# Performance work log

Hardware: AMD Instinct MI355X
Metric: run time of the kernel (lower is better)

Reference implementation:

```python
import jax, jax.numpy as jnp
import numpy as np

N, E, B, M = 50000, 100000, 50, 50
NPG = N // B            # atoms per graph
DIN, H1, H2, DE, AAF, G = 32, 32, 64, 16, 95, 128
K, T = 3, 6             # ARMA num_stacks, num_layers
F1, F2, F3 = 64, 32, 16
EA = 2 * (M - 1)        # amino-acid edges per graph


def setup_inputs() -> dict:
    key = jax.random.key(0)
    ks = jax.random.split(key, 24)
    s = 0.05
    def w(k, shape):
        return jax.random.normal(k, shape, jnp.float32) * s
    return {
        "x": jax.random.normal(ks[0], (N, DIN), jnp.float32),
        "edge_attr": jax.random.normal(ks[1], (E, DE), jnp.float32),
        "aa_features": jax.random.normal(ks[2], (B, M, AAF), jnp.float32),
        "edge_index": jax.random.randint(ks[3], (2, E), 0, N),
        "monomer_labels": jax.random.randint(ks[4], (B, NPG), 0, M),
        "amino_edge_index": jax.random.randint(ks[5], (2, EA), 0, M),
        "W_e1": w(ks[6], (DE, DIN * H1)), "b_e1": jnp.zeros((DIN * H1,), jnp.float32),
        "root1": w(ks[7], (DIN, H1)), "bias1": jnp.zeros((H1,), jnp.float32),
        "W_e2": w(ks[8], (DE, H1 * H2)), "b_e2": jnp.zeros((H1 * H2,), jnp.float32),
        "root2": w(ks[9], (H1, H2)), "bias2": jnp.zeros((H2,), jnp.float32),
        "Wa_atom": w(ks[10], (H2, 1)), "ba_atom": jnp.zeros((1,), jnp.float32),
        "arma_init_w": w(ks[11], (K, H2 + AAF, G)),
        "arma_w": w(ks[12], (T - 1, K, G, G)),
        "arma_root_w": w(ks[13], (T, K, H2 + AAF, G)),
        "arma_bias": jnp.zeros((T, K, G), jnp.float32),
        "Wa_aa": w(ks[14], (G, 1)), "ba_aa": jnp.zeros((1,), jnp.float32),
        "W1": w(ks[15], (G, F1)), "b1": jnp.zeros((F1,), jnp.float32),
        "W2": w(ks[16], (F1, F2)), "b2": jnp.zeros((F2,), jnp.float32),
        "W3": w(ks[17], (F2, F3)), "b3": jnp.zeros((F3,), jnp.float32),
        "W4": w(ks[18], (F3, 1)), "b4": jnp.zeros((1,), jnp.float32),
    }


def _nnconv(h, src, dst, edge_attr, Wm, bm, root, bias, fin, fout):
    # NNConv (aggr='add'): edge MLP -> per-edge weight matrix, gather-matmul-scatter
    w_e = (edge_attr @ Wm + bm).reshape(-1, fin, fout)            # [E, fin, fout]
    msg = jnp.einsum('ef,efo->eo', h[src], w_e)                   # [E, fout]
    agg = jax.ops.segment_sum(msg, dst, num_segments=h.shape[0])  # scatter-add to targets
    return agg + h @ root + bias


def _forward(x, edge_attr, aa_features, W_e1, b_e1, root1, bias1, W_e2, b_e2, root2, bias2,
             Wa_atom, ba_atom, arma_init_w, arma_w, arma_root_w, arma_bias, Wa_aa, ba_aa,
             W1, b1, W2, b2, W3, b3, W4, b4, edge_index, monomer_labels, amino_edge_index):
    src, dst = edge_index[0], edge_index[1]
    h = jax.nn.relu(_nnconv(x, src, dst, edge_attr, W_e1, b_e1, root1, bias1, DIN, H1))
    h = jax.nn.relu(_nnconv(h, src, dst, edge_attr, W_e2, b_e2, root2, bias2, H1, H2))

    # per-graph attention readout over atoms -> amino-acid embeddings (scatter by monomer label)
    xg = h.reshape(B, NPG, H2)
    attn = jax.nn.softmax(xg @ Wa_atom + ba_atom, axis=1)         # softmax over atoms in graph
    wx = xg * attn
    aa = jax.vmap(lambda wxi, lbl: jax.ops.segment_sum(wxi, lbl, num_segments=M))(wx, monomer_labels)
    h_aa = jnp.concatenate([aa, aa_features], axis=-1)            # [B, M, H2+95]

    # ARMAConv: gcn_norm without self-loops on amino-acid graph (shared across graphs)
    asrc, adst = amino_edge_index[0], amino_edge_index[1]
    deg = jax.ops.segment_sum(jnp.ones((EA,), x.dtype), adst, num_segments=M)
    dinv = jnp.where(deg > 0, 1.0 / jnp.sqrt(jnp.maximum(deg, 1.0)), 0.0)
    norm = dinv[asrc] * dinv[adst]                                # [EA]

    def arma(x0):  # x0: [M, H2+95]
        out = jnp.einsum('mf,kfo->kmo', x0, arma_init_w)          # [K, M, G]
        for t in range(T):
            if t > 0:
                out = jnp.einsum('kmo,kop->kmp', out, arma_w[t - 1])
            msg = out[:, asrc] * norm[None, :, None]              # [K, EA, G]
            prop = jax.vmap(lambda m: jax.ops.segment_sum(m, adst, num_segments=M))(msg)
            rootc = jnp.einsum('mf,kfo->kmo', x0, arma_root_w[t])
            out = jax.nn.relu(prop + rootc + arma_bias[t][:, None, :])
        return out.mean(axis=0)                                   # mean over stacks -> [M, G]

    g = jax.vmap(arma)(h_aa)                                      # [B, M, G]

    # attention readout over amino acids
    attn2 = jax.nn.softmax(g @ Wa_aa + ba_aa, axis=1)
    p = jnp.sum(g * attn2, axis=1)                                # [B, G]

    p = jax.nn.relu(p @ W1 + b1)
    p = jax.nn.relu(p @ W2 + b2)
    p = jax.nn.relu(p @ W3 + b3)
    p = p @ W4 + b4
    return p.reshape(-1)                                          # [B]


def reference(x, edge_attr, aa_features, edge_index, monomer_labels, amino_edge_index,
              W_e1, b_e1, root1, bias1, W_e2, b_e2, root2, bias2, Wa_atom, ba_atom,
              arma_init_w, arma_w, arma_root_w, arma_bias, Wa_aa, ba_aa,
              W1, b1, W2, b2, W3, b3, W4, b4):
    return _forward(x, edge_attr, aa_features, W_e1, b_e1, root1, bias1, W_e2, b_e2, root2, bias2,
                    Wa_atom, ba_atom, arma_init_w, arma_w, arma_root_w, arma_bias, Wa_aa, ba_aa,
                    W1, b1, W2, b2, W3, b3, W4, b4, edge_index, monomer_labels, amino_edge_index)
```

## Files before the change

### kernel.cpp

```cpp
#include <hip/hip_runtime.h>
#include <math.h>

#define N_ATOMS 50000
#define E_EDGES 100000
#define B_G     50
#define M_M     50
#define NPG     1000
#define DIN     32
#define H1C     32
#define H2C     64
#define DEC     16
#define AAF     95
#define G_DIM   128
#define K_ST    3
#define T_L     6
#define EA_E    98
#define XDIM    159
#define NS      21
#define MPAD    64
#define GP      132
#define GPS     136
#define KP2     168
#define KW      544
#define SLC     10
#define APB     100
#define NSB     ((N_ATOMS + 255) / 256)

#define OFF_WE2 (H1C * KW)
#define OFF_WT  (OFF_WE2 + H2C * KW)
#define OFF_AW  (OFF_WT + NS * XDIM * G_DIM)
#define OFF_DEG (OFF_AW + (T_L - 1) * K_ST * G_DIM * G_DIM)
#define PREP_TOTAL (OFF_DEG + E_EDGES)

typedef __attribute__((ext_vector_type(8))) short bf16x8;
typedef __attribute__((ext_vector_type(4))) float f32x4;
typedef __attribute__((ext_vector_type(4))) unsigned int u32x4;

__device__ __forceinline__ short f2bf(float f) {
    unsigned int u = __float_as_uint(f);
    unsigned int r = (u + 0x7FFFu + ((u >> 16) & 1u)) >> 16;
    return (short)r;
}
__device__ __forceinline__ float bf2f(short b) {
    return __uint_as_float(((unsigned int)(unsigned short)b) << 16);
}
__device__ __forceinline__ unsigned int cvtpk_bf16(float lo, float hi) {
    unsigned int r;
    asm("v_cvt_pk_bf16_f32 %0, %1, %2" : "=v"(r) : "v"(lo), "v"(hi));
    return r;
}

__device__ __forceinline__ void f4fma(float4& d, float s, const float4& v) {
    d.x += s * v.x; d.y += s * v.y; d.z += s * v.z; d.w += s * v.w;
}
__device__ __forceinline__ void f4add(float4& d, const float4& v) {
    d.x += v.x; d.y += v.y; d.z += v.z; d.w += v.w;
}
__device__ __forceinline__ void f4relu(float4& d) {
    d.x = fmaxf(d.x, 0.f); d.y = fmaxf(d.y, 0.f);
    d.z = fmaxf(d.z, 0.f); d.w = fmaxf(d.w, 0.f);
}

__global__ __launch_bounds__(256) void prep_all(
    const float* __restrict__ We1, const float* __restrict__ be1, short* __restrict__ WB1,
    const float* __restrict__ We2, const float* __restrict__ be2, short* __restrict__ WB2,
    const float* __restrict__ init_w, const float* __restrict__ root_w, short* __restrict__ Wtb,
    const float* __restrict__ arma_w, short* __restrict__ Wab,
    const int* __restrict__ eidx, int* __restrict__ deg,
    const int* __restrict__ aei, int* __restrict__ aa_off,
    int* __restrict__ aa_src, float* __restrict__ aa_nrm)
{
    int tid = threadIdx.x;
    if (blockIdx.x == 0) {
        __shared__ int   sdeg[M_M];
        __shared__ int   scur[M_M];
        __shared__ float sdinv[M_M];
        __shared__ int   soff[M_M + 1];
        if (tid < M_M) { sdeg[tid] = 0; scur[tid] = 0; }
        __syncthreads();
        if (tid < EA_E) atomicAdd(&sdeg[aei[EA_E + tid]], 1);
        __syncthreads();
        if (tid < M_M) {
            float dv = (float)sdeg[tid];
            sdinv[tid] = (dv > 0.f) ? (1.f / sqrtf(fmaxf(dv, 1.f))) : 0.f;
        }
        __syncthreads();
        if (tid == 0) {
            soff[0] = 0;
            for (int m = 0; m < M_M; ++m) soff[m + 1] = soff[m] + sdeg[m];
        }
        __syncthreads();
        if (tid < EA_E) {
            int ss = aei[tid], dd = aei[EA_E + tid];
            int pos = atomicAdd(&scur[dd], 1);
            int idx = soff[dd] + pos;
            aa_src[idx] = ss;
            aa_nrm[idx] = sdinv[ss] * sdinv[dd];
        }
        if (tid < M_M + 1) aa_off[tid] = soff[tid];
        return;
    }
    int idx = (blockIdx.x - 1) * 256 + tid;
    if (idx < OFF_WE2) {
        int o = idx / KW, k = idx - o * KW;
        float v = (k < 512) ? We1[(size_t)k * H1C + o]
                            : be1[(size_t)(k - 512) * H1C + o];
        WB1[idx] = f2bf(v);
    } else if (idx < OFF_WT) {
        int rem = idx - OFF_WE2;
        int o = rem / KW, k = rem - o * KW;
        float v = (k < 512) ? We2[(size_t)k * H2C + o]
                            : be2[(size_t)(k - 512) * H2C + o];
        WB2[rem] = f2bf(v);
    } else if (idx < OFF_AW) {
        int rem = idx - OFF_WT;
        int s = rem / (XDIM * G_DIM);
        int r2 = rem - s * XDIM * G_DIM;
        int k = r2 / G_DIM, n = r2 - k * G_DIM;
        float v = (s < K_ST) ? init_w[rem]
                             : root_w[(size_t)(s - K_ST) * XDIM * G_DIM + r2];
        Wtb[(size_t)s * G_DIM * KP2 + n * KP2 + k] = f2bf(v);
    } else if (idx < OFF_DEG) {
        int rem = idx - OFF_AW;
        int slot = rem / (G_DIM * G_DIM);
        int r2 = rem - slot * G_DIM * G_DIM;
        int p = r2 / G_DIM, n = r2 - p * G_DIM;
        Wab[(size_t)slot * G_DIM * G_DIM + n * G_DIM + p] = f2bf(arma_w[rem]);
    } else if (idx < PREP_TOTAL) {
        int e = idx - OFF_DEG;
        atomicAdd(&deg[eidx[E_EDGES + e]], 1);
    }
}

__global__ __launch_bounds__(256) void scan_part(const int* __restrict__ deg,
                                                 int* __restrict__ bsum)
{
    __shared__ int tmp[256];
    int tid = threadIdx.x;
    int n = blockIdx.x * 256 + tid;
    tmp[tid] = (n < N_ATOMS) ? deg[n] : 0;
    __syncthreads();
    for (int off = 128; off > 0; off >>= 1) {
        if (tid < off) tmp[tid] += tmp[tid + off];
        __syncthreads();
    }
    if (tid == 0) bsum[blockIdx.x] = tmp[0];
}

__global__ __launch_bounds__(256) void scan_mid(const int* __restrict__ bsum,
                                                int* __restrict__ bpre)
{
    __shared__ int tmp[256];
    int tid = threadIdx.x;
    int v = (tid < NSB) ? bsum[tid] : 0;
    tmp[tid] = v;
    __syncthreads();
    for (int off = 1; off < 256; off <<= 1) {
        int t = tmp[tid];
        int add = (tid >= off) ? tmp[tid - off] : 0;
        __syncthreads();
        tmp[tid] = t + add;
        __syncthreads();
    }
    if (tid < NSB) bpre[tid] = tmp[tid] - v;
}

__global__ __launch_bounds__(256) void scan_out(int* __restrict__ deg_off,
                                                const int* __restrict__ bpre)
{
    __shared__ int tmp[256];
    int tid = threadIdx.x;
    int n = blockIdx.x * 256 + tid;
    int v = (n < N_ATOMS) ? deg_off[n] : 0;
    tmp[tid] = v;
    __syncthreads();
    for (int off = 1; off < 256; off <<= 1) {
        int t = tmp[tid];
        int add = (tid >= off) ? tmp[tid - off] : 0;
        __syncthreads();
        tmp[tid] = t + add;
        __syncthreads();
    }
    int incl = tmp[tid];
    int base = bpre[blockIdx.x];
    if (n < N_ATOMS) deg_off[n] = base + incl - v;
    if (n == N_ATOMS - 1) deg_off[N_ATOMS] = base + incl;
}

template<int FOUT, int NTT, int WGRP, int MTB, bool CIPOS>
__global__ __launch_bounds__(256) void edge_msg_v2(
    const float* __restrict__ h, const float* __restrict__ ea,
    const int* __restrict__ eidx, int* __restrict__ ipos,
    const int* __restrict__ off, int* __restrict__ cursor,
    const short* __restrict__ WB, float* __restrict__ msg)
{
    constexpr int KS = 17;
    __shared__ int iplds[MTB * 16];
    int tid  = threadIdx.x;
    int lane = tid & 63, wave = tid >> 6;
    int l16  = lane & 15, quad = lane >> 4;
    int nt   = wave % NTT, tg = wave / NTT;
    int ebase = blockIdx.x * (MTB * 16);

    if (CIPOS) {
        if (tid < MTB * 16) {
            int e = ebase + tid;
            if (e < E_EDGES) {
                int d = eidx[E_EDGES + e];
                int pos = atomicAdd(&cursor[d], 1);
                int p = off[d] + pos;
                iplds[tid] = p;
                ipos[e] = p;
            }
        }
    }

    bf16x8 Bfr[KS];
    {
        const short* wb = WB + (size_t)(nt * 16 + l16) * KW;
        #pragma unroll
        for (int ks = 0; ks < KS; ++ks)
            Bfr[ks] = *(const bf16x8*)(wb + ks * 32 + quad * 8);
    }
    if (CIPOS) __syncthreads();

    for (int t = tg; t < MTB; t += WGRP) {
        int e  = ebase + t * 16 + l16;
        int es = (e < E_EDGES) ? e : (E_EDGES - 1);
        int s  = eidx[es];
        float4 h0 = *(const float4*)(h + (size_t)s * 32 + quad * 8);
        float4 h1 = *(const float4*)(h + (size_t)s * 32 + quad * 8 + 4);
        float hf[8] = {h0.x, h0.y, h0.z, h0.w, h1.x, h1.y, h1.z, h1.w};
        float4 e0 = *(const float4*)(ea + (size_t)es * DEC);
        float4 e1 = *(const float4*)(ea + (size_t)es * DEC + 4);
        float4 e2 = *(const float4*)(ea + (size_t)es * DEC + 8);
        float4 e3 = *(const float4*)(ea + (size_t)es * DEC + 12);
        float eaf[16] = {e0.x, e0.y, e0.z, e0.w, e1.x, e1.y, e1.z, e1.w,
                         e2.x, e2.y, e2.z, e2.w, e3.x, e3.y, e3.z, e3.w};

        f32x4 acc = (f32x4){0.f, 0.f, 0.f, 0.f};
        #pragma unroll
        for (int ks = 0; ks < KS; ++ks) {
            u32x4 av;
            if (ks < DEC) {
                float fac = eaf[ks];
                #pragma unroll
                for (int j = 0; j < 4; ++j)
                    av[j] = cvtpk_bf16(fac * hf[2 * j], fac * hf[2 * j + 1]);
            } else {
                #pragma unroll
                for (int j = 0; j < 4; ++j)
                    av[j] = cvtpk_bf16(hf[2 * j], hf[2 * j + 1]);
            }
            bf16x8 a = __builtin_bit_cast(bf16x8, av);
            acc = __builtin_amdgcn_mfma_f32_16x16x32_bf16(a, Bfr[ks], acc, 0, 0, 0);
        }
        int erb = ebase + t * 16 + quad * 4;
        #pragma unroll
        for (int r = 0; r < 4; ++r) {
            int ee = erb + r;
            if (ee < E_EDGES) {
                int p = CIPOS ? iplds[t * 16 + quad * 4 + r] : ipos[ee];
                msg[(size_t)p * FOUT + nt * 16 + l16] = acc[r];
            }
        }
    }
}

template<int FIN, int FOUT, bool SCORE>
__global__ __launch_bounds__(256) void gather_update(
    const float* __restrict__ msg, const int* __restrict__ off,
    const float* __restrict__ hin,
    const float* __restrict__ root, const float* __restrict__ bias,
    float* __restrict__ hout,
    const float* __restrict__ wa, const float* __restrict__ ba,
    float* __restrict__ sc)
{
    constexpr int NPB = 256 / FOUT;
    __shared__ float rlds[FIN][FOUT];
    __shared__ float hlds[NPB][FIN];
    int tid = threadIdx.x;
    for (int i = tid; i < FIN * FOUT / 4; i += 256) {
        *(float4*)&rlds[0][i * 4] = *(const float4*)(root + i * 4);
    }
    int nb = blockIdx.x * NPB;
    for (int i = tid; i < NPB * FIN; i += 256) {
        int ln = i / FIN, f = i % FIN;
        int n = nb + ln;
        hlds[ln][f] = (n < N_ATOMS) ? hin[(size_t)n * FIN + f] : 0.f;
    }
    __syncthreads();

    int ln = tid / FOUT, o = tid % FOUT;
    int n = nb + ln;
    if (n >= N_ATOMS) return;
    float acc = bias[o];
    #pragma unroll 8
    for (int f = 0; f < FIN; ++f) acc += hlds[ln][f] * rlds[f][o];
    int j0 = off[n], j1 = off[n + 1];
    for (int j = j0; j < j1; ++j) {
        acc += msg[(size_t)j * FOUT + o];
    }
    float hv = fmaxf(acc, 0.f);
    hout[(size_t)n * FOUT + o] = hv;
    if constexpr (SCORE) {
        static_assert(FOUT == 64, "score fusion needs node==wave");
        float sv = hv * wa[o];
        #pragma unroll
        for (int d = 32; d > 0; d >>= 1) sv += __shfl_down(sv, d);
        if (o == 0) sc[n] = sv + ba[0];
    }
}

__global__ __launch_bounds__(256) void atom_scatter_sm(
    const float* __restrict__ h2, const float* __restrict__ sc,
    const int* __restrict__ labels, float* __restrict__ partial)
{
    __shared__ float aa4[4][M_M][H2C];
    __shared__ float red[256];
    int b = blockIdx.x / SLC, s = blockIdx.x % SLC;
    int tid = threadIdx.x;
    int wave = tid >> 6, lane = tid & 63;
    const float* sb = sc + (size_t)b * NPG;

    for (int i = tid; i < 4 * M_M * H2C; i += 256) ((float*)aa4)[i] = 0.f;

    float lmax = -1e30f;
    for (int n = tid; n < NPG; n += 256) lmax = fmaxf(lmax, sb[n]);
    red[tid] = lmax;
    __syncthreads();
    for (int off = 128; off > 0; off >>= 1) {
        if (tid < off) red[tid] = fmaxf(red[tid], red[tid + off]);
        __syncthreads();
    }
    float mx = red[0];
    __syncthreads();
    float lsum = 0.f;
    for (int n = tid; n < NPG; n += 256) lsum += expf(sb[n] - mx);
    red[tid] = lsum;
    __syncthreads();
    for (int off = 128; off > 0; off >>= 1) {
        if (tid < off) red[tid] += red[tid + off];
        __syncthreads();
    }
    float inv = 1.f / red[0];
    __syncthreads();

    int nbase = s * APB;
    const float* hb = h2 + (size_t)b * NPG * H2C;
    #pragma unroll 5
    for (int it = 0; it < APB / 4; ++it) {
        int n = nbase + it * 4 + wave;
        int lbl = labels[b * NPG + n];
        float w = expf(sb[n] - mx) * inv;
        float hv = hb[(size_t)n * H2C + lane];
        aa4[wave][lbl][lane] += hv * w;
    }
    __syncthreads();
    float* pb = partial + (size_t)(b * SLC + s) * M_M * H2C;
    for (int i = tid; i < M_M * H2C; i += 256) {
        float v = ((float*)aa4)[i] + ((float*)aa4)[M_M * H2C + i]
                + ((float*)aa4)[2 * M_M * H2C + i] + ((float*)aa4)[3 * M_M * H2C + i];
        pb[i] = v;
    }
}

__global__ __launch_bounds__(256) void x0_finalize(
    const float* __restrict__ partial, const float* __restrict__ aaf,
    short* __restrict__ x0b)
{
    int idx = blockIdx.x * 256 + threadIdx.x;
    if (idx >= B_G * MPAD * KP2) return;
    int b = idx / (MPAD * KP2);
    int rem = idx - b * (MPAD * KP2);
    int m = rem / KP2, k = rem - m * KP2;
    float v = 0.f;
    if (m < M_M) {
        if (k < H2C) {
            const float* pb = partial + (size_t)b * SLC * M_M * H2C + m * H2C + k;
            #pragma unroll
            for (int s = 0; s < SLC; ++s) v += pb[(size_t)s * (M_M * H2C)];
        } else if (k < XDIM) {
            v = aaf[((size_t)b * M_M + m) * AAF + (k - H2C)];
        }
    }
    x0b[idx] = f2bf(v);
}

__global__ __launch_bounds__(256) void rc_gemm_mfma(
    const short* __restrict__ x0b, const short* __restrict__ Wtb,
    float* __restrict__ RC)
{
    int b = blockIdx.x / NS, s = blockIdx.x % NS;
    int tid = threadIdx.x;
    int lane = tid & 63, wave = tid >> 6;
    int l16 = lane & 15, quad = lane >> 4;
    const short* xa = x0b + (size_t)b * MPAD * KP2 + (wave * 16 + l16) * KP2;
    const short* wb = Wtb + (size_t)s * G_DIM * KP2;

    f32x4 acc[8];
    #pragma unroll
    for (int nt = 0; nt < 8; ++nt) acc[nt] = (f32x4){0.f, 0.f, 0.f, 0.f};

    #pragma unroll
    for (int ks = 0; ks < 5; ++ks) {
        bf16x8 a = *(const bf16x8*)(xa + ks * 32 + quad * 8);
        #pragma unroll
        for (int nt = 0; nt < 8; ++nt) {
            bf16x8 bf = *(const bf16x8*)(wb + (nt * 16 + l16) * KP2 + ks * 32 + quad * 8);
            acc[nt] = __builtin_amdgcn_mfma_f32_16x16x32_bf16(a, bf, acc[nt], 0, 0, 0);
        }
    }
    float* op = RC + (size_t)(b * NS + s) * M_M * G_DIM;
    #pragma unroll
    for (int nt = 0; nt < 8; ++nt) {
        #pragma unroll
        for (int r = 0; r < 4; ++r) {
            int m = wave * 16 + quad * 4 + r;
            if (m < M_M)
                op[m * G_DIM + nt * 16 + l16] = acc[nt][r];
        }
    }
}

__global__ __launch_bounds__(512) void arma_iter(
    const float* __restrict__ RC, const short* __restrict__ Wab,
    const float* __restrict__ arma_bias,
    const int* __restrict__ aa_off, const int* __restrict__ aa_src,
    const float* __restrict__ aa_nrm, float* __restrict__ gfull)
{
    __shared__ float Abuf[MPAD][GP];
    __shared__ float Bbuf[MPAD][GP];
    __shared__ short Bb16[MPAD][GPS];
    __shared__ int   s_off[M_M + 1];
    __shared__ int   s_src[EA_E];
    __shared__ float s_nrm[EA_E];
    int b = blockIdx.x / K_ST, k = blockIdx.x % K_ST;
    int tid = threadIdx.x;
    int oi = tid & 15, mi = tid >> 4;
    int c0 = oi * 4, c1 = 64 + oi * 4;
    int lane = tid & 63, wave = tid >> 6;
    int l16 = lane & 15, quad = lane >> 4;
    int mt = wave >> 1, nh = wave & 1;

    const float* rcb = RC + (size_t)b * NS * M_M * G_DIM;
    if (tid < M_M + 1) s_off[tid] = aa_off[tid];
    if (tid < EA_E) { s_src[tid] = aa_src[tid]; s_nrm[tid] = aa_nrm[tid]; }

    for (int i = tid; i < MPAD * G_DIM; i += 512) {
        int m = i >> 7, o = i & 127;
        Abuf[m][o] = (m < M_M) ? rcb[(size_t)k * M_M * G_DIM + i] : 0.f;
    }
    for (int i = tid; i < MPAD * GPS / 2; i += 512) {
        ((int*)Bb16)[i] = 0;
    }
    __syncthreads();

    for (int t = 0; t < T_L; ++t) {
        if (t > 0) {
            const short* aw = Wab + (size_t)((t - 1) * K_ST + k) * G_DIM * G_DIM;
            f32x4 acc[4];
            #pragma unroll
            for (int nt = 0; nt < 4; ++nt) acc[nt] = (f32x4){0.f, 0.f, 0.f, 0.f};
            #pragma unroll
            for (int ks = 0; ks < 4; ++ks) {
                bf16x8 a = *(const bf16x8*)&Bb16[mt * 16 + l16][ks * 32 + quad * 8];
                #pragma unroll
                for (int nt = 0; nt < 4; ++nt) {
                    int n0 = (nh * 4 + nt) * 16 + l16;
                    bf16x8 bf = *(const bf16x8*)(aw + n0 * G_DIM + ks * 32 + quad * 8);
                    acc[nt] = __builtin_amdgcn_mfma_f32_16x16x32_bf16(a, bf, acc[nt], 0, 0, 0);
                }
            }
            #pragma unroll
            for (int nt = 0; nt < 4; ++nt) {
                #pragma unroll
                for (int r = 0; r < 4; ++r) {
                    Abuf[mt * 16 + quad * 4 + r][(nh * 4 + nt) * 16 + l16] = acc[nt][r];
                }
            }
            __syncthreads();
        }
        const float* rct = rcb + (size_t)(K_ST + t * K_ST + k) * M_M * G_DIM;
        const float* bb  = arma_bias + ((size_t)t * K_ST + k) * G_DIM;
        float4 bias0 = *(const float4*)(bb + c0);
        float4 bias1 = *(const float4*)(bb + c1);
        #pragma unroll
        for (int r = 0; r < 2; ++r) {
            int m = mi * 2 + r;
            if (m < M_M) {
                const float* rr = rct + (size_t)m * G_DIM;
                float4 v0 = bias0, v1 = bias1;
                f4add(v0, *(const float4*)(rr + c0));
                f4add(v1, *(const float4*)(rr + c1));
                int j0 = s_off[m], j1 = s_off[m + 1];
                for (int j = j0; j < j1; ++j) {
                    float nv = s_nrm[j];
                    const float* ap = &Abuf[s_src[j]][0];
                    f4fma(v0, nv, *(const float4*)(ap + c0));
                    f4fma(v1, nv, *(const float4*)(ap + c1));
                }
                f4relu(v0);
                f4relu(v1);
                *(float4*)&Bbuf[m][c0] = v0;
                *(float4*)&Bbuf[m][c1] = v1;
                unsigned int p0 = cvtpk_bf16(v0.x, v0.y);
                unsigned int p1 = cvtpk_bf16(v0.z, v0.w);
                unsigned int p2 = cvtpk_bf16(v1.x, v1.y);
                unsigned int p3 = cvtpk_bf16(v1.z, v1.w);
                *(uint2*)&Bb16[m][c0] = make_uint2(p0, p1);
                *(uint2*)&Bb16[m][c1] = make_uint2(p2, p3);
            }
        }
        __syncthreads();
    }
    float* gb = gfull + ((size_t)(b * K_ST + k)) * M_M * G_DIM;
    for (int i = tid; i < M_M * G_DIM; i += 512) {
        int m = i >> 7, o = i & 127;
        gb[i] = Bbuf[m][o];
    }
}

__global__ __launch_bounds__(128) void aa_readout_mlp(
    const float* __restrict__ gfull, const float* __restrict__ wa,
    const float* __restrict__ ba,
    const float* __restrict__ W1, const float* __restrict__ b1,
    const float* __restrict__ W2, const float* __restrict__ b2,
    const float* __restrict__ W3, const float* __restrict__ b3,
    const float* __restrict__ W4, const float* __restrict__ b4,
    float* __restrict__ out)
{
    __shared__ float g[M_M][G_DIM + 1];
    __shared__ float s2[M_M];
    __shared__ float p[G_DIM];
    __shared__ float r1[64], r2[32], r3[16];
    int b = blockIdx.x, tid = threadIdx.x;
    const float* g0 = gfull + (size_t)b * K_ST * M_M * G_DIM;
    for (int i = tid; i < M_M * G_DIM; i += 128) {
        int m = i >> 7, o = i & 127;
        g[m][o] = (g0[i] + g0[M_M*G_DIM + i] + g0[2*M_M*G_DIM + i]) * (1.f/3.f);
    }
    __syncthreads();
    if (tid < M_M) {
        float sv = ba[0];
        for (int o = 0; o < G_DIM; ++o) sv += g[tid][o] * wa[o];
        s2[tid] = sv;
    }
    __syncthreads();
    if (tid == 0) {
        float mx = -1e30f;
        for (int m = 0; m < M_M; ++m) mx = fmaxf(mx, s2[m]);
        float den = 0.f;
        for (int m = 0; m < M_M; ++m) den += expf(s2[m] - mx);
        float inv = 1.f / den;
        for (int m = 0; m < M_M; ++m) s2[m] = expf(s2[m] - mx) * inv;
    }
    __syncthreads();
    {
        float pv = 0.f;
        for (int m = 0; m < M_M; ++m) pv += g[m][tid] * s2[m];
        p[tid] = pv;
    }
    __syncthreads();
    if (tid < 64) {
        float v = b1[tid];
        for (int i = 0; i < 128; ++i) v += p[i] * W1[i * 64 + tid];
        r1[tid] = fmaxf(v, 0.f);
    }
    __syncthreads();
    if (tid < 32) {
        float v = b2[tid];
        for (int i = 0; i < 64; ++i) v += r1[i] * W2[i * 32 + tid];
        r2[tid] = fmaxf(v, 0.f);
    }
    __syncthreads();
    if (tid < 16) {
        float v = b3[tid];
        for (int i = 0; i < 32; ++i) v += r2[i] * W3[i * 16 + tid];
        r3[tid] = fmaxf(v, 0.f);
    }
    __syncthreads();
    if (tid == 0) {
        float v = b4[0];
        for (int i = 0; i < 16; ++i) v += r3[i] * W4[i];
        out[b] = v;
    }
}

extern "C" void kernel_launch(void* const* d_in, const int* in_sizes, int n_in,
                              void* d_out, int out_size, void* d_ws, size_t ws_size,
                              hipStream_t stream)
{
    (void)in_sizes; (void)n_in; (void)out_size; (void)ws_size;
    const float* x            = (const float*)d_in[0];
    const float* edge_attr    = (const float*)d_in[1];
    const float* aa_features  = (const float*)d_in[2];
    const int*   edge_index   = (const int*)  d_in[3];
    const int*   mono_labels  = (const int*)  d_in[4];
    const int*   amino_ei     = (const int*)  d_in[5];
    const float* W_e1 = (const float*)d_in[6];
    const float* b_e1 = (const float*)d_in[7];
    const float* root1= (const float*)d_in[8];
    const float* bias1= (const float*)d_in[9];
    const float* W_e2 = (const float*)d_in[10];
    const float* b_e2 = (const float*)d_in[11];
    const float* root2= (const float*)d_in[12];
    const float* bias2= (const float*)d_in[13];
    const float* Wa_atom = (const float*)d_in[14];
    const float* ba_atom = (const float*)d_in[15];
    const float* arma_init_w = (const float*)d_in[16];
    const float* arma_w      = (const float*)d_in[17];
    const float* arma_root_w = (const float*)d_in[18];
    const float* arma_bias   = (const float*)d_in[19];
    const float* Wa_aa = (const float*)d_in[20];
    const float* ba_aa = (const float*)d_in[21];
    const float* W1 = (const float*)d_in[22];
    const float* b1 = (const float*)d_in[23];
    const float* W2 = (const float*)d_in[24];
    const float* b2 = (const float*)d_in[25];
    const float* W3 = (const float*)d_in[26];
    const float* b3 = (const float*)d_in[27];
    const float* W4 = (const float*)d_in[28];
    const float* b4 = (const float*)d_in[29];

    float* ws = (float*)d_ws;
    float* h1    = ws;
    float* h2    = h1   + (size_t)N_ATOMS * H1C;
    float* h_aa  = h2   + (size_t)N_ATOMS * H2C;
    float* sc    = h_aa + (size_t)B_G * M_M * XDIM;
    int*   aa_off = (int*)(sc + (size_t)B_G * NPG);
    int*   aa_src = aa_off + (M_M + 1);
    float* aa_nrm = (float*)(aa_src + EA_E);
    int*   deg_off = (int*)(aa_nrm + EA_E);
    int*   cursor  = deg_off + (N_ATOMS + 1);
    int*   ipos    = cursor + N_ATOMS;
    int*   bsum    = ipos + E_EDGES;
    int*   bpre    = bsum + 256;
    float* RC    = (float*)(bpre + 256);
    float* gfull = RC + (size_t)B_G * NS * M_M * G_DIM;
    short* Wtb   = (short*)((((uintptr_t)(gfull + (size_t)B_G * K_ST * M_M * G_DIM)) + 15)
                            & ~(uintptr_t)15);
    short* x0b   = Wtb + (size_t)NS * G_DIM * KP2;
    short* Wab   = x0b + (size_t)B_G * MPAD * KP2;
    short* WB1   = Wab + (size_t)(T_L - 1) * K_ST * G_DIM * G_DIM;
    short* WB2   = WB1 + (size_t)H1C * KW;
    float* msg   = RC;
    float* partial = RC;
    (void)h_aa;

    (void)hipMemsetAsync(deg_off, 0, (2 * N_ATOMS + 1) * sizeof(int), stream);

    prep_all<<<1 + (PREP_TOTAL + 255) / 256, 256, 0, stream>>>(
        W_e1, b_e1, WB1, W_e2, b_e2, WB2,
        arma_init_w, arma_root_w, Wtb, arma_w, Wab,
        edge_index, deg_off, amino_ei, aa_off, aa_src, aa_nrm);

    scan_part<<<NSB, 256, 0, stream>>>(deg_off, bsum);
    scan_mid<<<1, 256, 0, stream>>>(bsum, bpre);
    scan_out<<<NSB, 256, 0, stream>>>(deg_off, bpre);

    edge_msg_v2<H1C, 2, 2, 8, true><<<(E_EDGES + 127) / 128, 256, 0, stream>>>(
        x, edge_attr, edge_index, ipos, deg_off, cursor, WB1, msg);
    gather_update<DIN, H1C, false><<<(N_ATOMS + 7) / 8, 256, 0, stream>>>(
        msg, deg_off, x, root1, bias1, h1, nullptr, nullptr, nullptr);
    edge_msg_v2<H2C, 4, 1, 4, false><<<(E_EDGES + 63) / 64, 256, 0, stream>>>(
        h1, edge_attr, edge_index, ipos, nullptr, nullptr, WB2, msg);
    gather_update<H1C, H2C, true><<<(N_ATOMS + 3) / 4, 256, 0, stream>>>(
        msg, deg_off, h1, root2, bias2, h2, Wa_atom, ba_atom, sc);

    atom_scatter_sm<<<B_G * SLC, 256, 0, stream>>>(h2, sc, mono_labels, partial);
    x0_finalize<<<(B_G * MPAD * KP2 + 255) / 256, 256, 0, stream>>>(
        partial, aa_features, x0b);

    rc_gemm_mfma<<<B_G * NS, 256, 0, stream>>>(x0b, Wtb, RC);
    arma_iter<<<B_G * K_ST, 512, 0, stream>>>(RC, Wab, arma_bias,
                                              aa_off, aa_src, aa_nrm, gfull);
    aa_readout_mlp<<<B_G, 128, 0, stream>>>(gfull, Wa_aa, ba_aa, W1, b1, W2, b2, W3, b3, W4, b4,
                                            (float*)d_out);
}
```

Before: 315.2 us.

## Fuse root/init GEMM into ARMA iteration kernel and retune edge message tiling

Removes the separate rc_gemm_mfma launch and computes the initial and per-layer root projections of x0 inside arma_iter with MFMA, keeping x0 A-fragments in registers and writing results to a new shared Rbuf. This avoids writing and re-reading the large RC intermediate through global memory and saves a kernel launch. The cost is extra shared memory (another 64x132 float buffer, which may lower occupancy) and more serial work per block, since only 150 blocks now do all the GEMMs. The second edge message kernel also moves from 64 to 128 edges per block.

```diff
diff --git a/kernel.cpp b/kernel.cpp
--- a/kernel.cpp
+++ b/kernel.cpp
@@ -387,50 +387,15 @@
     x0b[idx] = f2bf(v);
 }
 
-__global__ __launch_bounds__(256) void rc_gemm_mfma(
+__global__ __launch_bounds__(512) void arma_iter(
     const short* __restrict__ x0b, const short* __restrict__ Wtb,
-    float* __restrict__ RC)
-{
-    int b = blockIdx.x / NS, s = blockIdx.x % NS;
-    int tid = threadIdx.x;
-    int lane = tid & 63, wave = tid >> 6;
-    int l16 = lane & 15, quad = lane >> 4;
-    const short* xa = x0b + (size_t)b * MPAD * KP2 + (wave * 16 + l16) * KP2;
-    const short* wb = Wtb + (size_t)s * G_DIM * KP2;
-
-    f32x4 acc[8];
-    #pragma unroll
-    for (int nt = 0; nt < 8; ++nt) acc[nt] = (f32x4){0.f, 0.f, 0.f, 0.f};
-
-    #pragma unroll
-    for (int ks = 0; ks < 5; ++ks) {
-        bf16x8 a = *(const bf16x8*)(xa + ks * 32 + quad * 8);
-        #pragma unroll
-        for (int nt = 0; nt < 8; ++nt) {
-            bf16x8 bf = *(const bf16x8*)(wb + (nt * 16 + l16) * KP2 + ks * 32 + quad * 8);
-            acc[nt] = __builtin_amdgcn_mfma_f32_16x16x32_bf16(a, bf, acc[nt], 0, 0, 0);
-        }
-    }
-    float* op = RC + (size_t)(b * NS + s) * M_M * G_DIM;
-    #pragma unroll
-    for (int nt = 0; nt < 8; ++nt) {
-        #pragma unroll
-        for (int r = 0; r < 4; ++r) {
-            int m = wave * 16 + quad * 4 + r;
-            if (m < M_M)
-                op[m * G_DIM + nt * 16 + l16] = acc[nt][r];
-        }
-    }
-}
-
-__global__ __launch_bounds__(512) void arma_iter(
-    const float* __restrict__ RC, const short* __restrict__ Wab,
-    const float* __restrict__ arma_bias,
+    const short* __restrict__ Wab, const float* __restrict__ arma_bias,
     const int* __restrict__ aa_off, const int* __restrict__ aa_src,
     const float* __restrict__ aa_nrm, float* __restrict__ gfull)
 {
     __shared__ float Abuf[MPAD][GP];
     __shared__ float Bbuf[MPAD][GP];
+    __shared__ float Rbuf[MPAD][GP];
     __shared__ short Bb16[MPAD][GPS];
     __shared__ int   s_off[M_M + 1];
     __shared__ int   s_src[EA_E];
@@ -443,18 +408,43 @@
     int l16 = lane & 15, quad = lane >> 4;
     int mt = wave >> 1, nh = wave & 1;
 
-    const float* rcb = RC + (size_t)b * NS * M_M * G_DIM;
     if (tid < M_M + 1) s_off[tid] = aa_off[tid];
     if (tid < EA_E) { s_src[tid] = aa_src[tid]; s_nrm[tid] = aa_nrm[tid]; }
-
-    for (int i = tid; i < MPAD * G_DIM; i += 512) {
-        int m = i >> 7, o = i & 127;
-        Abuf[m][o] = (m < M_M) ? rcb[(size_t)k * M_M * G_DIM + i] : 0.f;
-    }
     for (int i = tid; i < MPAD * GPS / 2; i += 512) {
         ((int*)Bb16)[i] = 0;
     }
-    __syncthreads();
+
+    bf16x8 Afr[5];
+    {
+        const short* xb = x0b + (size_t)b * MPAD * KP2 + (mt * 16 + l16) * KP2;
+        #pragma unroll
+        for (int ks = 0; ks < 5; ++ks)
+            Afr[ks] = *(const bf16x8*)(xb + ks * 32 + quad * 8);
+    }
+
+    auto x0_gemm = [&](const short* __restrict__ W, float (*dst)[GP]) {
+        f32x4 acc[4];
+        #pragma unroll
+        for (int nt = 0; nt < 4; ++nt) acc[nt] = (f32x4){0.f, 0.f, 0.f, 0.f};
+        #pragma unroll
+        for (int ks = 0; ks < 5; ++ks) {
+            #pragma unroll
+            for (int nt = 0; nt < 4; ++nt) {
+                int n0 = (nh * 4 + nt) * 16 + l16;
+                bf16x8 bf = *(const bf16x8*)(W + (size_t)n0 * KP2 + ks * 32 + quad * 8);
+                acc[nt] = __builtin_amdgcn_mfma_f32_16x16x32_bf16(Afr[ks], bf, acc[nt], 0, 0, 0);
+            }
+        }
+        #pragma unroll
+        for (int nt = 0; nt < 4; ++nt) {
+            #pragma unroll
+            for (int r = 0; r < 4; ++r) {
+                dst[mt * 16 + quad * 4 + r][(nh * 4 + nt) * 16 + l16] = acc[nt][r];
+            }
+        }
+    };
+
+    x0_gemm(Wtb + (size_t)k * G_DIM * KP2, Abuf);
 
     for (int t = 0; t < T_L; ++t) {
         if (t > 0) {
@@ -479,20 +469,20 @@
                     Abuf[mt * 16 + quad * 4 + r][(nh * 4 + nt) * 16 + l16] = acc[nt][r];
                 }
             }
-            __syncthreads();
-        }
-        const float* rct = rcb + (size_t)(K_ST + t * K_ST + k) * M_M * G_DIM;
-        const float* bb  = arma_bias + ((size_t)t * K_ST + k) * G_DIM;
+        }
+        x0_gemm(Wtb + (size_t)(K_ST + t * K_ST + k) * G_DIM * KP2, Rbuf);
+        __syncthreads();
+
+        const float* bb = arma_bias + ((size_t)t * K_ST + k) * G_DIM;
         float4 bias0 = *(const float4*)(bb + c0);
         float4 bias1 = *(const float4*)(bb + c1);
         #pragma unroll
         for (int r = 0; r < 2; ++r) {
             int m = mi * 2 + r;
             if (m < M_M) {
-                const float* rr = rct + (size_t)m * G_DIM;
                 float4 v0 = bias0, v1 = bias1;
-                f4add(v0, *(const float4*)(rr + c0));
-                f4add(v1, *(const float4*)(rr + c1));
+                f4add(v0, *(const float4*)&Rbuf[m][c0]);
+                f4add(v1, *(const float4*)&Rbuf[m][c1]);
                 int j0 = s_off[m], j1 = s_off[m + 1];
                 for (int j = j0; j < j1; ++j) {
                     float nv = s_nrm[j];
@@ -663,7 +653,7 @@
         x, edge_attr, edge_index, ipos, deg_off, cursor, WB1, msg);
     gather_update<DIN, H1C, false><<<(N_ATOMS + 7) / 8, 256, 0, stream>>>(
         msg, deg_off, x, root1, bias1, h1, nullptr, nullptr, nullptr);
-    edge_msg_v2<H2C, 4, 1, 4, false><<<(E_EDGES + 63) / 64, 256, 0, stream>>>(
+    edge_msg_v2<H2C, 4, 1, 8, false><<<(E_EDGES + 127) / 128, 256, 0, stream>>>(
         h1, edge_attr, edge_index, ipos, nullptr, nullptr, WB2, msg);
     gather_update<H1C, H2C, true><<<(N_ATOMS + 3) / 4, 256, 0, stream>>>(
         msg, deg_off, h1, root2, bias2, h2, Wa_atom, ba_atom, sc);
@@ -672,8 +662,7 @@
     x0_finalize<<<(B_G * MPAD * KP2 + 255) / 256, 256, 0, stream>>>(
         partial, aa_features, x0b);
 
-    rc_gemm_mfma<<<B_G * NS, 256, 0, stream>>>(x0b, Wtb, RC);
-    arma_iter<<<B_G * K_ST, 512, 0, stream>>>(RC, Wab, arma_bias,
+    arma_iter<<<B_G * K_ST, 512, 0, stream>>>(x0b, Wtb, Wab, arma_bias,
                                               aa_off, aa_src, aa_nrm, gfull);
     aa_readout_mlp<<<B_G, 128, 0, stream>>>(gfull, Wa_aa, ba_aa, W1, b1, W2, b2, W3, b3, W4, b4,
                                             (float*)d_out);
```

New measurement: 305.2 us. 1.03x faster.
